# Kernel tuning notes

Hardware: AMD Instinct MI355X
Metric: run time of the kernel (lower is better)

## Reference

```python
import jax, jax.numpy as jnp
import numpy as np

S = 1            # support_num
NEIGHBOR = 32    # neighbor_num for ball query
EPS = 1e-12

def _gather(t, idx):
    # t: (bs, N, C), idx: (bs, M, n) -> (bs, M, n, C)
    return jax.vmap(lambda tb, ib: tb[ib])(t, idx)

def _pick(t, idx):
    # t: (bs, M, C), idx: (bs, V) -> (bs, V, C)
    return jax.vmap(lambda tb, ib: tb[ib])(t, idx)

def _normalize(x, axis):
    return x / jnp.maximum(jnp.linalg.norm(x, axis=axis, keepdims=True), EPS)

def query_ball_point(radius, nsample, xyz, new_xyz):
    # PointNet++-style ball query: indices of first nsample points within radius,
    # missing slots filled with the first valid neighbor (self, since dist=0).
    sq = jnp.sum((new_xyz[:, :, None, :] - xyz[:, None, :, :]) ** 2, axis=-1)  # (bs,S,N)
    N = xyz.shape[1]
    idx = jnp.broadcast_to(jnp.arange(N), sq.shape)
    idx = jnp.where(sq > radius * radius, N, idx)
    idx = jnp.sort(idx, axis=-1)[:, :, :nsample]
    return jnp.where(idx == N, idx[:, :, :1], idx)

def _dir_norm(vertices, nbr_idx):
    nbrs = _gather(vertices, nbr_idx)                       # (bs,v,n,3)
    return _normalize(nbrs - vertices[:, :, None, :], axis=-1)

def conv_surface(nbr_idx, vertices, directions, K=32):
    # directions: (3, S*K)
    dn = _dir_norm(vertices, nbr_idx)
    theta = jax.nn.relu(jnp.einsum('bvnd,dk->bvnk', dn, _normalize(directions, 0)))
    bs, v, n, _ = theta.shape
    return theta.reshape(bs, v, n, S, K).max(axis=2).sum(axis=2)  # (bs,v,K)

def conv_layer(nbr_idx, vertices, fm, w, b, d, K=32):
    # w: (Cin,(S+1)*K), b: ((S+1)*K,), d: (3,S*K)
    dn = _dir_norm(vertices, nbr_idx)
    theta = jax.nn.relu(jnp.einsum('bvnd,dk->bvnk', dn, _normalize(d, 0)))  # (bs,v,n,S*K)
    f = jnp.einsum('bvc,ck->bvk', fm, w) + b                # (bs,v,(S+1)*K)
    center, support = f[..., :K], f[..., K:]
    sup = _gather(support, nbr_idx)                          # (bs,v,n,S*K)
    bs, v, n, _ = sup.shape
    act = (theta * sup).reshape(bs, v, n, S, K).max(axis=2).sum(axis=2)
    return center + act

def pool_layer(vertices, fm, radius, key, rate=4, nn_num=4):
    idx = query_ball_point(radius, nn_num, vertices, vertices)
    pooled = _gather(fm, idx).max(axis=2)                    # neighborhood max-pool
    v = vertices.shape[1]
    perm = jax.random.permutation(key, v)[: v // rate]       # random subsample (fixed key)
    return vertices[:, perm], pooled[:, perm]

def get_nearest_index(target, source):
    sq = jnp.sum((target[:, :, None, :] - source[:, None, :, :]) ** 2, axis=-1)
    return jnp.argmin(sq, axis=-1)                           # (bs, V_target)

def _forward(vertices, onehot, d0, w1, b1, dd1, w2, b2, dd2, w3, b3, dd3,
             w4, b4, dd4, w5, b5, dd5, w6, b6, dd6, w7, b7, dd7,
             cw1, cb1, cw2, cb2, cw3, cb3):
    relu = jax.nn.relu
    bs, V, _ = vertices.shape
    ni = query_ball_point(0.25, NEIGHBOR, vertices, vertices)
    fm0 = relu(conv_surface(ni, vertices, d0))
    fm1 = jnp.concatenate([fm0, relu(conv_layer(ni, vertices, fm0, w1, b1, dd1))], -1)
    fm2 = jnp.concatenate([fm1, relu(conv_layer(ni, vertices, fm1, w2, b2, dd2))], -1)
    v1, fp1 = pool_layer(vertices, fm2, 0.25, jax.random.fold_in(jax.random.key(42), 1))
    ni = query_ball_point(0.39, NEIGHBOR, v1, v1)
    fm3 = jnp.concatenate([fp1, relu(conv_layer(ni, v1, fp1, w3, b3, dd3))], -1)
    fm4 = jnp.concatenate([fm3, relu(conv_layer(ni, v1, fm3, w4, b4, dd4))], -1)
    fm5 = jnp.concatenate([fm4, relu(conv_layer(ni, v1, fm4, w5, b5, dd5))], -1)
    v2, fp2 = pool_layer(v1, fm5, 0.39, jax.random.fold_in(jax.random.key(42), 2))
    ni = query_ball_point(0.63, NEIGHBOR, v2, v2)
    fm6 = jnp.concatenate([fp2, relu(conv_layer(ni, v2, fp2, w6, b6, dd6))], -1)
    fm7 = jnp.concatenate([fm6, relu(conv_layer(ni, v2, fm6, w7, b7, dd7))], -1)
    f_global = fm7.max(axis=1)                               # (bs, 256)
    n1 = get_nearest_index(vertices, v1)
    n2 = get_nearest_index(vertices, v2)
    fuse = jnp.concatenate([
        fm0, fm1, fm2,
        _pick(fm3, n1), _pick(fm4, n1), _pick(fm5, n1),
        _pick(fm6, n2), _pick(fm7, n2),
        jnp.broadcast_to(f_global[:, None, :], (bs, V, f_global.shape[-1])),
        jnp.broadcast_to(onehot[:, None, :], (bs, V, onehot.shape[-1])),
    ], axis=-1)                                              # (bs, V, 1424)
    h = relu(jnp.einsum('bvc,oc->bvo', fuse, cw1) + cb1)
    h = relu(jnp.einsum('bvc,oc->bvo', h, cw2) + cb2)
    return jnp.einsum('bvc,oc->bvo', h, cw3) + cb3           # (bs, V, class_num)


def setup_inputs() -> dict:
    key = jax.random.key(0)
    ks = iter(jax.random.split(key, 40))
    bs, N, cat = 8, 2048, 16
    vertices = jax.random.uniform(next(ks), (bs, N, 3), dtype=jnp.float32)
    labels = jax.random.randint(next(ks), (bs,), 0, cat)
    onehot = jax.nn.one_hot(labels, cat, dtype=jnp.float32)
    def p(shape):
        return jax.random.normal(next(ks), shape, dtype=jnp.float32) * 0.05
    inp = {"vertices": vertices, "onehot": onehot, "d0": p((3, S * 32))}
    ins = [32, 64, 96, 128, 160, 192, 224]
    for i, c in enumerate(ins, start=1):
        inp[f"w{i}"] = p((c, (S + 1) * 32))
        inp[f"b{i}"] = p(((S + 1) * 32,))
        inp[f"dd{i}"] = p((3, S * 32))
    inp["cw1"] = p((1024, 1424)); inp["cb1"] = p((1024,))
    inp["cw2"] = p((512, 1024)); inp["cb2"] = p((512,))
    inp["cw3"] = p((50, 512)); inp["cb3"] = p((50,))
    return inp


def reference(vertices, onehot, d0, w1, b1, dd1, w2, b2, dd2, w3, b3, dd3,
              w4, b4, dd4, w5, b5, dd5, w6, b6, dd6, w7, b7, dd7,
              cw1, cb1, cw2, cb2, cw3, cb3):
    return _forward(vertices, onehot, d0, w1, b1, dd1, w2, b2, dd2, w3, b3, dd3,
                    w4, b4, dd4, w5, b5, dd5, w6, b6, dd6, w7, b7, dd7,
                    cw1, cb1, cw2, cb2, cw3, cb3)
```

## Files before the change

### kernel.cpp

```cpp
#include <hip/hip_runtime.h>
#include <hip/hip_bf16.h>

#define BS 8
#define V0 2048
#define V1N 512
#define V2N 128

typedef unsigned short ushort_t;
typedef __attribute__((ext_vector_type(8))) short bf16x8;
typedef __attribute__((ext_vector_type(4))) float f32x4;

__device__ __forceinline__ void tf2x32(unsigned k0, unsigned k1,
                                       unsigned x0, unsigned x1,
                                       unsigned &o0, unsigned &o1) {
  unsigned ks2 = k0 ^ k1 ^ 0x1BD11BDAu;
  x0 += k0; x1 += k1;
#define RR(r) { x0 += x1; x1 = (x1 << (r)) | (x1 >> (32 - (r))); x1 ^= x0; }
  RR(13) RR(15) RR(26) RR(6)   x0 += k1;  x1 += ks2 + 1u;
  RR(17) RR(29) RR(16) RR(24)  x0 += ks2; x1 += k0 + 2u;
  RR(13) RR(15) RR(26) RR(6)   x0 += k0;  x1 += k1 + 3u;
  RR(17) RR(29) RR(16) RR(24)  x0 += k1;  x1 += ks2 + 4u;
  RR(13) RR(15) RR(26) RR(6)   x0 += ks2; x1 += k0 + 5u;
#undef RR
  o0 = x0; o1 = x1;
}

__device__ __forceinline__ ushort_t f2bf(float f) {
  unsigned u = __float_as_uint(f);
  u += 0x7FFFu + ((u >> 16) & 1u);
  return (ushort_t)(u >> 16);
}

__device__ __forceinline__ float sqdist_f32(float cx, float cy, float cz,
                                            const float* p) {
  float dx = __fsub_rn(cx, p[0]);
  float dy = __fsub_rn(cy, p[1]);
  float dz = __fsub_rn(cz, p[2]);
  return __fadd_rn(__fadd_rn(__fmul_rn(dx, dx), __fmul_rn(dy, dy)),
                   __fmul_rn(dz, dz));
}

#define KP1 1472

#define PREP_BLKS 8193
__global__ __launch_bounds__(256) void misc1_kernel(
    int* __restrict__ rank, const float* __restrict__ cw1,
    const float* __restrict__ cw2, const float* __restrict__ cw3,
    const float* __restrict__ cb3, ushort_t* __restrict__ cw1b,
    ushort_t* __restrict__ cw2b, ushort_t* __restrict__ cw3b,
    float* __restrict__ cb3p, const float* __restrict__ pts,
    int* __restrict__ ni1) {
  int bid = blockIdx.x, tid = threadIdx.x;
  if (bid < 18) {
    __shared__ unsigned sb[2048];
    int seg, segfirst, n, base;
    if (bid < 8)       { seg = 0; segfirst = 0;  n = 2048; base = 0; }
    else if (bid < 16) { seg = 1; segfirst = 8;  n = 2048; base = 2048; }
    else               { seg = 2; segfirst = 16; n = 512;  base = 4096; }
    unsigned k0, k1, nk0, nk1, sk0, sk1;
    if (seg == 0) {
      tf2x32(0u, 42u, 0u, 1u, k0, k1);
      tf2x32(k0, k1, 0u, 1u, sk0, sk1);
    } else if (seg == 1) {
      tf2x32(0u, 42u, 0u, 1u, k0, k1);
      tf2x32(k0, k1, 0u, 0u, nk0, nk1);
      tf2x32(nk0, nk1, 0u, 1u, sk0, sk1);
    } else {
      tf2x32(0u, 42u, 0u, 2u, k0, k1);
      tf2x32(k0, k1, 0u, 1u, sk0, sk1);
    }
    for (int i = tid; i < n; i += 256) {
      unsigned o0, o1;
      tf2x32(sk0, sk1, 0u, (unsigned)i, o0, o1);
      sb[i] = o0 ^ o1;
    }
    __syncthreads();
    int tt = (bid - segfirst) * 256 + tid;
    unsigned bt = sb[tt];
    int cnt = 0;
#pragma unroll 8
    for (int s = 0; s < n; ++s) {
      unsigned bs = sb[s];
      cnt += (bs < bt) || (bs == bt && s < tt);
    }
    rank[base + tt] = cnt;
  } else if (bid < 18 + PREP_BLKS) {
    long long t = (long long)(bid - 18) * 256 + tid;
    const long long N1 = 1024LL * KP1, N2 = 512LL * 1024, N3 = 128LL * 512;
    if (t < N1) {
      int k = (int)(t % KP1);
      int n = (int)(t / KP1);
      cw1b[t] = f2bf(k < 1424 ? cw1[(size_t)n * 1424 + k] : 0.f);
    } else if (t < N1 + N2) {
      long long u = t - N1;
      cw2b[u] = f2bf(cw2[u]);
    } else if (t < N1 + N2 + N3) {
      long long u = t - N1 - N2;
      int k = (int)(u & 511);
      int n = (int)(u >> 9);
      cw3b[u] = f2bf(n < 50 ? cw3[(size_t)n * 512 + k] : 0.f);
    } else if (t < N1 + N2 + N3 + 128) {
      int u = (int)(t - N1 - N2 - N3);
      cb3p[u] = u < 50 ? cb3[u] : 0.f;
    }
  } else {
    int bq = bid - 18 - PREP_BLKS;
    int wid = bq * 4 + (tid >> 6);
    int lane = tid & 63;
    int b = wid >> 11, i = wid & 2047;
    const float* base = pts + (size_t)b * V0 * 3;
    float cx = base[i * 3], cy = base[i * 3 + 1], cz = base[i * 3 + 2];
    int cnt = 0, idx0 = 0;
    for (int j0 = 0; j0 < V0; j0 += 64) {
      int j = j0 + lane;
      float d2 = sqdist_f32(cx, cy, cz, base + (size_t)j * 3);
      bool in = (d2 <= 0.0625f);
      unsigned long long mask = __ballot(in);
      if (cnt == 0 && mask) idx0 = j0 + __builtin_ctzll(mask);
      if (in) {
        int rk = cnt + __popcll(mask & ((1ull << lane) - 1ull));
        if (rk < 32) ni1[(size_t)wid * 32 + rk] = j;
      }
      cnt += __popcll(mask);
      if (cnt >= 32) break;
    }
    for (int s = cnt + lane; s < 32; s += 64) ni1[(size_t)wid * 32 + s] = idx0;
  }
}

__device__ __forceinline__ void dirn(const float* base, int v, int nb,
                                     float& ox, float& oy, float& oz) {
  float dx = __fsub_rn(base[nb * 3 + 0], base[v * 3 + 0]);
  float dy = __fsub_rn(base[nb * 3 + 1], base[v * 3 + 1]);
  float dz = __fsub_rn(base[nb * 3 + 2], base[v * 3 + 2]);
  float s2 = __fadd_rn(__fadd_rn(__fmul_rn(dx, dx), __fmul_rn(dy, dy)),
                       __fmul_rn(dz, dz));
  float nrm = fmaxf(__fsqrt_rn(s2), 1e-12f);
  ox = __fdiv_rn(dx, nrm); oy = __fdiv_rn(dy, nrm); oz = __fdiv_rn(dz, nrm);
}

__device__ __forceinline__ void norm_col(const float* d, int k,
                                         float& ox, float& oy, float& oz) {
  float x = d[k], y = d[32 + k], z = d[64 + k];
  float s2 = __fadd_rn(__fadd_rn(__fmul_rn(x, x), __fmul_rn(y, y)),
                       __fmul_rn(z, z));
  float nrm = fmaxf(__fsqrt_rn(s2), 1e-12f);
  ox = __fdiv_rn(x, nrm); oy = __fdiv_rn(y, nrm); oz = __fdiv_rn(z, nrm);
}

__global__ __launch_bounds__(256) void misc2_kernel(
    const int* __restrict__ rank, int* __restrict__ perm1,
    int* __restrict__ perm2, const float* __restrict__ pts,
    const int* __restrict__ ni, const float* __restrict__ d0,
    const float* __restrict__ w1, const float* __restrict__ b1,
    float* __restrict__ out, float* __restrict__ fn) {
  int bid = blockIdx.x, tid = threadIdx.x;
  if (bid == 0) {
    __shared__ int a1[2048];
    __shared__ int a2[2048];
    for (int i = tid; i < 2048; i += 256) a1[rank[i]] = i;
    __syncthreads();
    for (int i = tid; i < 2048; i += 256) a2[rank[2048 + i]] = a1[i];
    __syncthreads();
    for (int i = tid; i < 512; i += 256) perm1[i] = a2[i];
    for (int i = tid; i < 512; i += 256) a1[rank[4096 + i]] = i;
    __syncthreads();
    for (int i = tid; i < 128; i += 256) perm2[i] = a1[i];
    return;
  }
  __shared__ float sdir[3][32];
  __shared__ float sdn[8][32][3];
  __shared__ float sfm[8][32];
  if (tid < 32) {
    float x, y, z; norm_col(d0, tid, x, y, z);
    sdir[0][tid] = x; sdir[1][tid] = y; sdir[2][tid] = z;
  }
  int vloc = tid >> 5, k = tid & 31;
  size_t bvg = (size_t)(bid - 1) * 8 + vloc;
  int b = (int)(bvg >> 11), v = (int)(bvg & 2047);
  const float* base = pts + (size_t)b * V0 * 3;
  int nb = ni[bvg * 32 + k];
  float x, y, z; dirn(base, v, nb, x, y, z);
  sdn[vloc][k][0] = x; sdn[vloc][k][1] = y; sdn[vloc][k][2] = z;
  __syncthreads();
  float m = 0.f;
  for (int n = 0; n < 32; ++n) {
    float d = sdn[vloc][n][0] * sdir[0][k] + sdn[vloc][n][1] * sdir[1][k] +
              sdn[vloc][n][2] * sdir[2][k];
    m = fmaxf(m, fmaxf(d, 0.f));
  }
  out[bvg * 96 + k] = m;
  sfm[vloc][k] = m;
  __syncthreads();
  float a1v = b1[k], a2v = b1[k + 32];
  for (int c = 0; c < 32; ++c) {
    float vv = sfm[vloc][c];
    a1v += vv * w1[c * 64 + k];
    a2v += vv * w1[c * 64 + k + 32];
  }
  fn[bvg * 64 + k] = a1v;
  fn[bvg * 64 + k + 32] = a2v;
}

__global__ __launch_bounds__(256) void conv_act_kernel(
    const float* __restrict__ pts, const float* __restrict__ dd,
    const int* __restrict__ ni, const float* __restrict__ f,
    float* __restrict__ out, int Nv, int ldout, int colofs,
    const float* __restrict__ wn, const float* __restrict__ bn,
    float* __restrict__ fn) {
  __shared__ float sdir[3][32];
  __shared__ float sdn[8][32][3];
  __shared__ int sidx[8][32];
  __shared__ float sfm[8][256];
  int tid = threadIdx.x;
  if (tid < 32) {
    float x, y, z; norm_col(dd, tid, x, y, z);
    sdir[0][tid] = x; sdir[1][tid] = y; sdir[2][tid] = z;
  }
  int vloc = tid >> 5, k = tid & 31;
  size_t bvg = (size_t)blockIdx.x * 8 + vloc;
  int b = (int)(bvg / Nv), v = (int)(bvg % Nv);
  const float* base = pts + (size_t)b * Nv * 3;
  int nb = ni[bvg * 32 + k];
  float x, y, z; dirn(base, v, nb, x, y, z);
  sdn[vloc][k][0] = x; sdn[vloc][k][1] = y; sdn[vloc][k][2] = z;
  sidx[vloc][k] = nb;
  __syncthreads();
  float m = -INFINITY;
  size_t fb = (size_t)b * Nv * 64;
  for (int n = 0; n < 32; ++n) {
    float th = fmaxf(sdn[vloc][n][0] * sdir[0][k] + sdn[vloc][n][1] * sdir[1][k] +
                     sdn[vloc][n][2] * sdir[2][k], 0.f);
    float sup = f[fb + (size_t)sidx[vloc][n] * 64 + 32 + k];
    m = fmaxf(m, th * sup);
  }
  float center = f[bvg * 64 + k];
  float res = fmaxf(center + m, 0.f);
  out[bvg * ldout + colofs + k] = res;
  if (wn) {
    size_t rowbase = (size_t)blockIdx.x * 8;
#pragma unroll 1
    for (int r = 0; r < 8; ++r)
      if (tid < colofs) sfm[r][tid] = out[(rowbase + r) * ldout + tid];
    sfm[vloc][colofs + k] = res;
    __syncthreads();
    int cin = colofs + 32;
    float a1v = bn[k], a2v = bn[k + 32];
    for (int c = 0; c < cin; ++c) {
      float vv = sfm[vloc][c];
      a1v += vv * wn[c * 64 + k];
      a2v += vv * wn[c * 64 + k + 32];
    }
    fn[bvg * 64 + k] = a1v;
    fn[bvg * 64 + k + 32] = a2v;
  }
}

__global__ __launch_bounds__(256) void conv_act_qbp_kernel(
    const float* __restrict__ pts, int Nv, float rrq,
    const float* __restrict__ dd, int* __restrict__ ni_out,
    const float* __restrict__ f, float* __restrict__ out, int ldout,
    int colofs, const float* __restrict__ wn, const float* __restrict__ bn,
    float* __restrict__ fn) {
  __shared__ float spts[512 * 3];
  __shared__ float sdir[3][32];
  __shared__ float sdn[8][32][3];
  __shared__ int sni[8][32];
  __shared__ float sfm[8][256];
  int tid = threadIdx.x;
  int b = (blockIdx.x * 8) / Nv;
  int vbase = (blockIdx.x * 8) % Nv;
  const float* gp = pts + (size_t)b * Nv * 3;
  for (int i = tid; i < Nv * 3; i += 256) spts[i] = gp[i];
  if (tid < 32) {
    float x, y, z; norm_col(dd, tid, x, y, z);
    sdir[0][tid] = x; sdir[1][tid] = y; sdir[2][tid] = z;
  }
  __syncthreads();
  int lane = tid & 63, wv = tid >> 6;
  for (int rep = 0; rep < 2; ++rep) {
    int vl = wv * 2 + rep;
    int v = vbase + vl;
    float cx = spts[v * 3], cy = spts[v * 3 + 1], cz = spts[v * 3 + 2];
    int cnt = 0, idx0 = 0;
    for (int j0 = 0; j0 < Nv; j0 += 64) {
      int j = j0 + lane;
      float d2 = sqdist_f32(cx, cy, cz, spts + (size_t)j * 3);
      bool in = (d2 <= rrq);
      unsigned long long mask = __ballot(in);
      if (cnt == 0 && mask) idx0 = j0 + __builtin_ctzll(mask);
      if (in) {
        int rk = cnt + __popcll(mask & ((1ull << lane) - 1ull));
        if (rk < 32) sni[vl][rk] = j;
      }
      cnt += __popcll(mask);
      if (cnt >= 32) break;
    }
    for (int s = cnt + lane; s < 32; s += 64) sni[vl][s] = idx0;
  }
  __syncthreads();
  ni_out[(size_t)(blockIdx.x * 8) * 32 + tid] = sni[tid >> 5][tid & 31];
  int vloc = tid >> 5, k = tid & 31;
  size_t bvg = (size_t)blockIdx.x * 8 + vloc;
  int v = vbase + vloc;
  int nb = sni[vloc][k];
  float x, y, z; dirn(spts, v, nb, x, y, z);
  sdn[vloc][k][0] = x; sdn[vloc][k][1] = y; sdn[vloc][k][2] = z;
  __syncthreads();
  float m = -INFINITY;
  size_t fb = (size_t)b * Nv * 64;
  for (int n = 0; n < 32; ++n) {
    float th = fmaxf(sdn[vloc][n][0] * sdir[0][k] + sdn[vloc][n][1] * sdir[1][k] +
                     sdn[vloc][n][2] * sdir[2][k], 0.f);
    float sup = f[fb + (size_t)sni[vloc][n] * 64 + 32 + k];
    m = fmaxf(m, th * sup);
  }
  float center = f[bvg * 64 + k];
  float res = fmaxf(center + m, 0.f);
  out[bvg * ldout + colofs + k] = res;
  size_t rowbase = (size_t)blockIdx.x * 8;
#pragma unroll 1
  for (int r = 0; r < 8; ++r)
    if (tid < colofs) sfm[r][tid] = out[(rowbase + r) * ldout + tid];
  sfm[vloc][colofs + k] = res;
  __syncthreads();
  int cin = colofs + 32;
  float a1v = bn[k], a2v = bn[k + 32];
  for (int c = 0; c < cin; ++c) {
    float vv = sfm[vloc][c];
    a1v += vv * wn[c * 64 + k];
    a2v += vv * wn[c * 64 + k + 32];
  }
  fn[bvg * 64 + k] = a1v;
  fn[bvg * 64 + k + 32] = a2v;
}

__global__ __launch_bounds__(256) void pool_kernel(
    const float* __restrict__ pts_in, const float* __restrict__ fm_in,
    int ld_in, int C, int Nv_in, const int* __restrict__ perm, int Nv_out,
    float rr, float* __restrict__ pts_out, float* __restrict__ fm_out,
    int ld_out, const float* __restrict__ wn, const float* __restrict__ bn,
    float* __restrict__ fn) {
  __shared__ float spf[4][192];
  int wv = threadIdx.x >> 6;
  int lane = threadIdx.x & 63;
  int wid = blockIdx.x * 4 + wv;
  int b = wid / Nv_out, pp = wid - b * Nv_out;
  int v = perm[pp];
  const float* base = pts_in + (size_t)b * Nv_in * 3;
  float cx = base[v * 3], cy = base[v * 3 + 1], cz = base[v * 3 + 2];
  int nb[4]; int cnt = 0;
  for (int j0 = 0; j0 < Nv_in && cnt < 4; j0 += 64) {
    int j = j0 + lane;
    float d2 = sqdist_f32(cx, cy, cz, base + (size_t)j * 3);
    unsigned long long mask = __ballot(d2 <= rr);
    while (mask && cnt < 4) {
      int bp = __builtin_ctzll(mask);
      mask &= mask - 1;
      nb[cnt++] = j0 + bp;
    }
  }
  for (int q = cnt; q < 4; ++q) nb[q] = nb[0];
  if (lane < 3) pts_out[(size_t)wid * 3 + lane] = base[v * 3 + lane];
  size_t inrow = (size_t)b * Nv_in;
  size_t outrow = (size_t)wid * ld_out;
  for (int c = lane; c < C; c += 64) {
    float m = fm_in[(inrow + nb[0]) * ld_in + c];
    m = fmaxf(m, fm_in[(inrow + nb[1]) * ld_in + c]);
    m = fmaxf(m, fm_in[(inrow + nb[2]) * ld_in + c]);
    m = fmaxf(m, fm_in[(inrow + nb[3]) * ld_in + c]);
    fm_out[outrow + c] = m;
    spf[wv][c] = m;
  }
  __syncthreads();
  int o = threadIdx.x & 63, w_ = threadIdx.x >> 6;
  int wid0 = blockIdx.x * 4 + w_;
  float a = bn[o];
  for (int c = 0; c < C; ++c) a += spf[w_][c] * wn[c * 64 + o];
  fn[(size_t)wid0 * 64 + o] = a;
}

__global__ void gmax_kernel(const float* __restrict__ fm,
                            float* __restrict__ out) {
  int t = blockIdx.x * blockDim.x + threadIdx.x;
  if (t >= BS * 256) return;
  int b = t >> 8, c = t & 255;
  float m = -INFINITY;
  for (int v = 0; v < V2N; ++v)
    m = fmaxf(m, fm[((size_t)b * V2N + v) * 256 + c]);
  out[t] = m;
}

__global__ __launch_bounds__(256) void fuse_row_kernel(
    const float* __restrict__ fm2, const float* __restrict__ fm5,
    const float* __restrict__ fm7, const float* __restrict__ fglob,
    const float* __restrict__ onehot, const float* __restrict__ verts,
    const float* __restrict__ v1, const float* __restrict__ v2,
    ushort_t* __restrict__ fuse_b) {
  __shared__ unsigned long long red[256];
  __shared__ int sn1, sn2;
  int bv = blockIdx.x;
  int b = bv >> 11;
  int tid = threadIdx.x;
  float cx = verts[(size_t)bv * 3 + 0];
  float cy = verts[(size_t)bv * 3 + 1];
  float cz = verts[(size_t)bv * 3 + 2];
  unsigned long long best = ~0ull;
  const float* sb = v1 + (size_t)b * V1N * 3;
  for (int j = tid; j < V1N; j += 256) {
    float d2 = sqdist_f32(cx, cy, cz, sb + (size_t)j * 3);
    unsigned long long key =
        (((unsigned long long)__float_as_uint(d2)) << 32) | (unsigned)j;
    best = best < key ? best : key;
  }
  red[tid] = best;
  __syncthreads();
  for (int s = 128; s > 0; s >>= 1) {
    if (tid < s) red[tid] = red[tid] < red[tid + s] ? red[tid] : red[tid + s];
    __syncthreads();
  }
  if (tid == 0) sn1 = (int)(red[0] & 0xffffffffu);
  __syncthreads();
  best = ~0ull;
  sb = v2 + (size_t)b * V2N * 3;
  for (int j = tid; j < V2N; j += 256) {
    float d2 = sqdist_f32(cx, cy, cz, sb + (size_t)j * 3);
    unsigned long long key =
        (((unsigned long long)__float_as_uint(d2)) << 32) | (unsigned)j;
    best = best < key ? best : key;
  }
  red[tid] = best;
  __syncthreads();
  for (int s = 128; s > 0; s >>= 1) {
    if (tid < s) red[tid] = red[tid] < red[tid + s] ? red[tid] : red[tid + s];
    __syncthreads();
  }
  if (tid == 0) sn2 = (int)(red[0] & 0xffffffffu);
  __syncthreads();
  const float* r2 = fm2 + (size_t)bv * 96;
  const float* r5 = fm5 + ((size_t)b * V1N + sn1) * 192;
  const float* r7 = fm7 + ((size_t)b * V2N + sn2) * 256;
  const float* rg = fglob + b * 256;
  const float* roh = onehot + b * 16;
  if (tid < KP1 / 8) {
    int c = tid * 8;
    const float* src = nullptr;
    if (c < 192) {
      int cc = (c < 32) ? c : (c < 96 ? c - 32 : c - 96);
      src = r2 + cc;
    } else if (c < 672) {
      int cc = (c < 320) ? c - 192 : (c < 480 ? c - 320 : c - 480);
      src = r5 + cc;
    } else if (c < 1152) {
      int cc = (c < 896) ? c - 672 : c - 896;
      src = r7 + cc;
    } else if (c < 1408) {
      src = rg + (c - 1152);
    } else if (c < 1424) {
      src = roh + (c - 1408);
    }
    float4 lo = make_float4(0.f, 0.f, 0.f, 0.f), hi = lo;
    if (src) { lo = *(const float4*)src; hi = *(const float4*)(src + 4); }
    bf16x8 o;
    o[0] = (short)f2bf(lo.x); o[1] = (short)f2bf(lo.y);
    o[2] = (short)f2bf(lo.z); o[3] = (short)f2bf(lo.w);
    o[4] = (short)f2bf(hi.x); o[5] = (short)f2bf(hi.y);
    o[6] = (short)f2bf(hi.z); o[7] = (short)f2bf(hi.w);
    *(bf16x8*)(fuse_b + (size_t)bv * KP1 + c) = o;
  }
}

typedef const __attribute__((address_space(1))) unsigned int gas_u32;
typedef __attribute__((address_space(3))) unsigned int las_u32;

__global__ __launch_bounds__(256) void gemm_mfma_nt(
    const ushort_t* __restrict__ A, const ushort_t* __restrict__ B,
    const float* __restrict__ bias, ushort_t* __restrict__ Cb,
    float* __restrict__ Cf, int K, int ldc, int nvalid, int mode) {
  __shared__ ushort_t As[128 * 64];
  __shared__ ushort_t Bs[128 * 64];
  int tid = threadIdx.x;
  int lane = tid & 63, w = tid >> 6;
  int wm = (w >> 1) * 64, wn = (w & 1) * 64;
  int nb = gridDim.x;
  int flat = blockIdx.x + nb * blockIdx.y;
  int xcd = flat & 7, slot = flat >> 3;
  int nidx = slot % nb;
  int mband = xcd + 8 * (slot / nb);
  int bm = mband * 128, bn = nidx * 128;
  f32x4 acc[4][4];
#pragma unroll
  for (int i = 0; i < 4; ++i)
#pragma unroll
    for (int j = 0; j < 4; ++j) acc[i][j] = (f32x4){0.f, 0.f, 0.f, 0.f};

  const ushort_t* gA[4];
  const ushort_t* gB[4];
  ushort_t* lA[4];
  ushort_t* lB[4];
  int rsub = lane >> 3;
  int scol = ((lane & 7) ^ rsub) * 8;
#pragma unroll
  for (int g = 0; g < 4; ++g) {
    int r = w * 32 + g * 8 + rsub;
    gA[g] = A + (size_t)(bm + r) * K + scol;
    gB[g] = B + (size_t)(bn + r) * K + scol;
    lA[g] = As + (w * 32 + g * 8) * 64;
    lB[g] = Bs + (w * 32 + g * 8) * 64;
  }
  int rA = lane & 15, q = lane >> 4;
  int r7 = rA & 7;

  for (int k0 = 0; k0 < K; k0 += 64) {
#pragma unroll
    for (int g = 0; g < 4; ++g)
      __builtin_amdgcn_global_load_lds((gas_u32*)(gA[g] + k0), (las_u32*)lA[g],
                                       16, 0, 0);
#pragma unroll
    for (int g = 0; g < 4; ++g)
      __builtin_amdgcn_global_load_lds((gas_u32*)(gB[g] + k0), (las_u32*)lB[g],
                                       16, 0, 0);
    __syncthreads();
#pragma unroll
    for (int s = 0; s < 2; ++s) {
      int pc = ((s * 4 + q) ^ r7) * 8;
      bf16x8 af[4], bfr[4];
#pragma unroll
      for (int i = 0; i < 4; ++i)
        af[i] = *(const bf16x8*)(As + (wm + i * 16 + rA) * 64 + pc);
#pragma unroll
      for (int j = 0; j < 4; ++j)
        bfr[j] = *(const bf16x8*)(Bs + (wn + j * 16 + rA) * 64 + pc);
#pragma unroll
      for (int i = 0; i < 4; ++i)
#pragma unroll
        for (int j = 0; j < 4; ++j)
          acc[i][j] = __builtin_amdgcn_mfma_f32_16x16x32_bf16(af[i], bfr[j],
                                                              acc[i][j], 0, 0, 0);
    }
    __syncthreads();
  }

  int rowq = (lane >> 4) * 4;
  int coll = lane & 15;
#pragma unroll
  for (int i = 0; i < 4; ++i) {
#pragma unroll
    for (int j = 0; j < 4; ++j) {
      int col = bn + wn + j * 16 + coll;
      float bi = bias[col];
#pragma unroll
      for (int r = 0; r < 4; ++r) {
        int row = bm + wm + i * 16 + rowq + r;
        float v = acc[i][j][r] + bi;
        if (mode == 0) {
          Cb[(size_t)row * ldc + col] = f2bf(fmaxf(v, 0.f));
        } else if (col < nvalid) {
          Cf[(size_t)row * ldc + col] = v;
        }
      }
    }
  }
}

__global__ __launch_bounds__(512, 2) void gemm256_mfma_nt(
    const ushort_t* __restrict__ A, const ushort_t* __restrict__ B,
    const float* __restrict__ bias, ushort_t* __restrict__ Cb,
    int K, int ldc) {
  __shared__ ushort_t As[2 * 256 * 64];
  __shared__ ushort_t Bs[2 * 256 * 64];
  int tid = threadIdx.x;
  int lane = tid & 63, w = tid >> 6;
  int wm = (w >> 2) * 128, wn = (w & 3) * 64;

  int flat = blockIdx.x;
  int xcd = flat & 7, slot = flat >> 3;
  int nidx = slot & 3, mband = xcd + 8 * (slot >> 2);
  int bm = mband * 256, bn = nidx * 256;

  f32x4 acc[8][4];
#pragma unroll
  for (int i = 0; i < 8; ++i)
#pragma unroll
    for (int j = 0; j < 4; ++j) acc[i][j] = (f32x4){0.f, 0.f, 0.f, 0.f};

  int rloc = tid >> 3, cch = tid & 7;
  int gc = (cch ^ (rloc & 7)) * 8;
  const ushort_t* gA[4];
  const ushort_t* gB[4];
#pragma unroll
  for (int i = 0; i < 4; ++i) {
    gA[i] = A + (size_t)(bm + i * 64 + rloc) * K + gc;
    gB[i] = B + (size_t)(bn + i * 64 + rloc) * K + gc;
  }
  int lofs = tid * 8;

  int rA = lane & 15, qlane = lane >> 4, r7 = lane & 7;
  int pc0 = (qlane ^ r7) * 8;
  int pc1 = ((4 + qlane) ^ r7) * 8;

  int NT = K >> 6;

#pragma unroll
  for (int i = 0; i < 4; ++i) {
    __builtin_amdgcn_global_load_lds((gas_u32*)gA[i],
                                     (las_u32*)(As + i * 4096 + lofs), 16, 0, 0);
    gA[i] += 64;
  }
#pragma unroll
  for (int i = 0; i < 4; ++i) {
    __builtin_amdgcn_global_load_lds((gas_u32*)gB[i],
                                     (las_u32*)(Bs + i * 4096 + lofs), 16, 0, 0);
    gB[i] += 64;
  }

  for (int t = 0; t < NT; ++t) {
    int doff = (t & 1) * 16384;
    int poff = doff ^ 16384;
    if (t + 1 < NT) {
#pragma unroll
      for (int i = 0; i < 4; ++i) {
        __builtin_amdgcn_global_load_lds(
            (gas_u32*)gA[i], (las_u32*)(As + poff + i * 4096 + lofs), 16, 0, 0);
        gA[i] += 64;
      }
#pragma unroll
      for (int i = 0; i < 4; ++i) {
        __builtin_amdgcn_global_load_lds(
            (gas_u32*)gB[i], (las_u32*)(Bs + poff + i * 4096 + lofs), 16, 0, 0);
        gB[i] += 64;
      }
      asm volatile("s_waitcnt vmcnt(8)" ::: "memory");
    } else {
      asm volatile("s_waitcnt vmcnt(0)" ::: "memory");
    }
    __builtin_amdgcn_sched_barrier(0);
    __builtin_amdgcn_s_barrier();
    __builtin_amdgcn_sched_barrier(0);

    const ushort_t* Ab = As + doff;
    const ushort_t* Bb = Bs + doff;
#pragma unroll
    for (int qd = 0; qd < 4; ++qd) {
      int qrow = (qd >> 1) * 64, qcol = (qd & 1) * 32;
      bf16x8 afr[2][4], bfr[2][2];
#pragma unroll
      for (int s = 0; s < 2; ++s) {
        int pcs = s ? pc1 : pc0;
#pragma unroll
        for (int fi = 0; fi < 4; ++fi)
          afr[s][fi] =
              *(const bf16x8*)(Ab + (wm + qrow + fi * 16 + rA) * 64 + pcs);
#pragma unroll
        for (int fj = 0; fj < 2; ++fj)
          bfr[s][fj] =
              *(const bf16x8*)(Bb + (wn + qcol + fj * 16 + rA) * 64 + pcs);
      }
      __builtin_amdgcn_s_setprio(1);
#pragma unroll
      for (int s = 0; s < 2; ++s)
#pragma unroll
        for (int fi = 0; fi < 4; ++fi)
#pragma unroll
          for (int fj = 0; fj < 2; ++fj) {
            int i = (qd >> 1) * 4 + fi, j = (qd & 1) * 2 + fj;
            acc[i][j] = __builtin_amdgcn_mfma_f32_16x16x32_bf16(
                afr[s][fi], bfr[s][fj], acc[i][j], 0, 0, 0);
          }
      __builtin_amdgcn_s_setprio(0);
      __builtin_amdgcn_sched_barrier(0);
      __builtin_amdgcn_s_barrier();
      __builtin_amdgcn_sched_barrier(0);
    }
  }

  int rowq = (lane >> 4) * 4;
  int coll = lane & 15;
  float bi[4];
#pragma unroll
  for (int j = 0; j < 4; ++j) bi[j] = bias[bn + wn + j * 16 + coll];
#pragma unroll
  for (int i = 0; i < 8; ++i) {
#pragma unroll
    for (int j = 0; j < 4; ++j) {
      int col = bn + wn + j * 16 + coll;
#pragma unroll
      for (int r = 0; r < 4; ++r) {
        int row = bm + wm + i * 16 + rowq + r;
        float v = acc[i][j][r] + bi[j];
        Cb[(size_t)row * ldc + col] = f2bf(fmaxf(v, 0.f));
      }
    }
  }
}

extern "C" void kernel_launch(void* const* d_in, const int* in_sizes, int n_in,
                              void* d_out, int out_size, void* d_ws,
                              size_t ws_size, hipStream_t stream) {
  const float* vertices = (const float*)d_in[0];
  const float* onehot = (const float*)d_in[1];
  const float* d0 = (const float*)d_in[2];
  const float *w[8], *bb[8], *dd[8];
  for (int i = 1; i <= 7; ++i) {
    w[i] = (const float*)d_in[3 * i];
    bb[i] = (const float*)d_in[3 * i + 1];
    dd[i] = (const float*)d_in[3 * i + 2];
  }
  const float* cw1 = (const float*)d_in[24];
  const float* cb1 = (const float*)d_in[25];
  const float* cw2 = (const float*)d_in[26];
  const float* cb2 = (const float*)d_in[27];
  const float* cw3 = (const float*)d_in[28];
  const float* cb3 = (const float*)d_in[29];
  float* out = (float*)d_out;

  char* wsp = (char*)d_ws;
  size_t off = 0;
  auto alloc = [&](size_t bytes) -> void* {
    void* p = wsp + off;
    off += (bytes + 255) & ~(size_t)255;
    return p;
  };
  const int M = BS * V0;
  int* rank = (int*)alloc(4608 * 4);
  int* perm1 = (int*)alloc(512 * 4);
  int* perm2 = (int*)alloc(128 * 4);
  int* ni1 = (int*)alloc((size_t)BS * V0 * 32 * 4);
  int* ni2 = (int*)alloc((size_t)BS * V1N * 32 * 4);
  int* ni3 = (int*)alloc((size_t)BS * V2N * 32 * 4);
  float* fm2buf = (float*)alloc((size_t)BS * V0 * 96 * 4);
  float* fm5buf = (float*)alloc((size_t)BS * V1N * 192 * 4);
  float* fm7buf = (float*)alloc((size_t)BS * V2N * 256 * 4);
  float* fbuf = (float*)alloc((size_t)BS * V0 * 64 * 4);
  float* v1 = (float*)alloc((size_t)BS * V1N * 3 * 4);
  float* v2 = (float*)alloc((size_t)BS * V2N * 3 * 4);
  float* fglob = (float*)alloc((size_t)BS * 256 * 4);
  ushort_t* fuse_b = (ushort_t*)alloc((size_t)M * KP1 * 2);
  ushort_t* h1b = (ushort_t*)alloc((size_t)M * 1024 * 2);
  ushort_t* h2b = (ushort_t*)alloc((size_t)M * 512 * 2);
  ushort_t* cw1b = (ushort_t*)alloc((size_t)1024 * KP1 * 2);
  ushort_t* cw2b = (ushort_t*)alloc((size_t)512 * 1024 * 2);
  ushort_t* cw3b = (ushort_t*)alloc((size_t)128 * 512 * 2);
  float* cb3p = (float*)alloc(128 * 4);

  float rr1 = 0.0625f;
  float rr2 = (float)(0.39 * 0.39);
  float rr3 = (float)(0.63 * 0.63);

  misc1_kernel<<<18 + PREP_BLKS + 4096, 256, 0, stream>>>(
      rank, cw1, cw2, cw3, cb3, cw1b, cw2b, cw3b, cb3p, vertices, ni1);
  misc2_kernel<<<1 + BS * V0 / 8, 256, 0, stream>>>(
      rank, perm1, perm2, vertices, ni1, d0, w[1], bb[1], fm2buf, fbuf);
  conv_act_kernel<<<BS * V0 / 8, 256, 0, stream>>>(
      vertices, dd[1], ni1, fbuf, fm2buf, V0, 96, 32, w[2], bb[2], fbuf);
  conv_act_kernel<<<BS * V0 / 8, 256, 0, stream>>>(
      vertices, dd[2], ni1, fbuf, fm2buf, V0, 96, 64, nullptr, nullptr, nullptr);
  pool_kernel<<<BS * V1N / 4, 256, 0, stream>>>(
      vertices, fm2buf, 96, 96, V0, perm1, V1N, rr1, v1, fm5buf, 192,
      w[3], bb[3], fbuf);
  conv_act_qbp_kernel<<<BS * V1N / 8, 256, 0, stream>>>(
      v1, V1N, rr2, dd[3], ni2, fbuf, fm5buf, 192, 96, w[4], bb[4], fbuf);
  conv_act_kernel<<<BS * V1N / 8, 256, 0, stream>>>(
      v1, dd[4], ni2, fbuf, fm5buf, V1N, 192, 128, w[5], bb[5], fbuf);
  conv_act_kernel<<<BS * V1N / 8, 256, 0, stream>>>(
      v1, dd[5], ni2, fbuf, fm5buf, V1N, 192, 160, nullptr, nullptr, nullptr);
  pool_kernel<<<BS * V2N / 4, 256, 0, stream>>>(
      v1, fm5buf, 192, 192, V1N, perm2, V2N, rr2, v2, fm7buf, 256,
      w[6], bb[6], fbuf);
  conv_act_qbp_kernel<<<BS * V2N / 8, 256, 0, stream>>>(
      v2, V2N, rr3, dd[6], ni3, fbuf, fm7buf, 256, 192, w[7], bb[7], fbuf);
  conv_act_kernel<<<BS * V2N / 8, 256, 0, stream>>>(
      v2, dd[7], ni3, fbuf, fm7buf, V2N, 256, 224, nullptr, nullptr, nullptr);
  gmax_kernel<<<BS, 256, 0, stream>>>(fm7buf, fglob);
  fuse_row_kernel<<<M, 256, 0, stream>>>(fm2buf, fm5buf, fm7buf, fglob, onehot,
                                         vertices, v1, v2, fuse_b);
  gemm256_mfma_nt<<<(M / 256) * (1024 / 256), 512, 0, stream>>>(
      fuse_b, cw1b, cb1, h1b, KP1, 1024);
  gemm_mfma_nt<<<dim3(512 / 128, M / 128), 256, 0, stream>>>(
      h1b, cw2b, cb2, h2b, nullptr, 1024, 512, 512, 0);
  gemm_mfma_nt<<<dim3(1, M / 128), 256, 0, stream>>>(
      h2b, cw3b, cb3p, nullptr, out, 512, 50, 50, 1);
}
```

Baseline: 416.0 us.

## Restructure GEMM k-loop: hoist B fragments, drop per-quadrant barriers, wait before prefetch

The bf16 MFMA GEMM main loop now loads all four B fragments once per k-tile and iterates over two A row bands, instead of four quadrants that each reload A and B fragments. The three per-quadrant workgroup barriers are removed. Synchronization moves to the top of each iteration: a full vmcnt(0) wait and a barrier before issuing the next tile's prefetch. This cuts LDS fragment reloads and barrier count, but the prefetch no longer overlaps with waiting on the current tile, so load latency may be exposed.

```diff
diff --git a/kernel.cpp b/kernel.cpp
--- a/kernel.cpp
+++ b/kernel.cpp
@@ -595,7 +595,8 @@
   }
   int lofs = tid * 8;
 
-  int rA = lane & 15, qlane = lane >> 4, r7 = lane & 7;
+  int rA = lane & 15, r7 = lane & 7;
+  int qlane = lane >> 4;
   int pc0 = (qlane ^ r7) * 8;
   int pc1 = ((4 + qlane) ^ r7) * 8;
 
@@ -617,6 +618,12 @@
   for (int t = 0; t < NT; ++t) {
     int doff = (t & 1) * 16384;
     int poff = doff ^ 16384;
+
+    asm volatile("s_waitcnt vmcnt(0)" ::: "memory");
+    __builtin_amdgcn_sched_barrier(0);
+    __builtin_amdgcn_s_barrier();
+    __builtin_amdgcn_sched_barrier(0);
+
     if (t + 1 < NT) {
 #pragma unroll
       for (int i = 0; i < 4; ++i) {
@@ -630,31 +637,27 @@
             (gas_u32*)gB[i], (las_u32*)(Bs + poff + i * 4096 + lofs), 16, 0, 0);
         gB[i] += 64;
       }
-      asm volatile("s_waitcnt vmcnt(8)" ::: "memory");
-    } else {
-      asm volatile("s_waitcnt vmcnt(0)" ::: "memory");
-    }
-    __builtin_amdgcn_sched_barrier(0);
-    __builtin_amdgcn_s_barrier();
-    __builtin_amdgcn_sched_barrier(0);
+    }
 
     const ushort_t* Ab = As + doff;
     const ushort_t* Bb = Bs + doff;
-#pragma unroll
-    for (int qd = 0; qd < 4; ++qd) {
-      int qrow = (qd >> 1) * 64, qcol = (qd & 1) * 32;
-      bf16x8 afr[2][4], bfr[2][2];
+    bf16x8 bfr[2][4];
+#pragma unroll
+    for (int s = 0; s < 2; ++s) {
+      int pcs = s ? pc1 : pc0;
+#pragma unroll
+      for (int fj = 0; fj < 4; ++fj)
+        bfr[s][fj] = *(const bf16x8*)(Bb + (wn + fj * 16 + rA) * 64 + pcs);
+    }
+#pragma unroll
+    for (int band = 0; band < 2; ++band) {
+      bf16x8 afr[2][4];
 #pragma unroll
       for (int s = 0; s < 2; ++s) {
         int pcs = s ? pc1 : pc0;
 #pragma unroll
         for (int fi = 0; fi < 4; ++fi)
-          afr[s][fi] =
-              *(const bf16x8*)(Ab + (wm + qrow + fi * 16 + rA) * 64 + pcs);
-#pragma unroll
-        for (int fj = 0; fj < 2; ++fj)
-          bfr[s][fj] =
-              *(const bf16x8*)(Bb + (wn + qcol + fj * 16 + rA) * 64 + pcs);
+          afr[s][fi] = *(const bf16x8*)(Ab + (wm + band * 64 + fi * 16 + rA) * 64 + pcs);
       }
       __builtin_amdgcn_s_setprio(1);
 #pragma unroll
@@ -662,16 +665,13 @@
 #pragma unroll
         for (int fi = 0; fi < 4; ++fi)
 #pragma unroll
-          for (int fj = 0; fj < 2; ++fj) {
-            int i = (qd >> 1) * 4 + fi, j = (qd & 1) * 2 + fj;
-            acc[i][j] = __builtin_amdgcn_mfma_f32_16x16x32_bf16(
-                afr[s][fi], bfr[s][fj], acc[i][j], 0, 0, 0);
-          }
+          for (int fj = 0; fj < 4; ++fj)
+            acc[band * 4 + fi][fj] = __builtin_amdgcn_mfma_f32_16x16x32_bf16(
+                afr[s][fi], bfr[s][fj], acc[band * 4 + fi][fj], 0, 0, 0);
       __builtin_amdgcn_s_setprio(0);
-      __builtin_amdgcn_sched_barrier(0);
-      __builtin_amdgcn_s_barrier();
-      __builtin_amdgcn_sched_barrier(0);
-    }
+    }
+    asm volatile("s_waitcnt lgkmcnt(0)" ::: "memory");
+    __builtin_amdgcn_sched_barrier(0);
   }
 
   int rowq = (lane >> 4) * 4;
```

After: 427.4 us. +2.7%, slower.
